# Optimization experiments

Hardware: AMD Instinct MI355X
Metric: run time of the kernel (lower is better)

The kernel has to match this reference:

```python
import jax, jax.numpy as jnp
import numpy as np

E = 16        # num_experts
H = 1024      # hidden_size
I = 768       # moe_intermediate_size
TOP_K = 2     # num_experts_per_tok
B, S = 1, 2048


def setup_inputs() -> dict:
    key = jax.random.key(0)
    ks = jax.random.split(key, 5)
    scale = 0.02
    return {
        "hidden_states": jax.random.normal(ks[0], (B, S, H), dtype=jnp.float32),
        "gate_w": jax.random.normal(ks[1], (E, H), dtype=jnp.float32) * scale,
        "gate_proj": jax.random.normal(ks[2], (E, I, H), dtype=jnp.float32) * scale,
        "up_proj": jax.random.normal(ks[3], (E, I, H), dtype=jnp.float32) * scale,
        "down_proj": jax.random.normal(ks[4], (E, H, I), dtype=jnp.float32) * scale,
    }


def reference(hidden_states, gate_w, gate_proj, up_proj, down_proj):
    b, s, h = hidden_states.shape
    x = hidden_states.reshape(-1, h)                        # [T, H]
    T = x.shape[0]

    # Router: logits -> fp32 softmax -> top-k -> renormalize (norm_topk_prob=True)
    router_logits = x @ gate_w.T                            # [T, E]
    probs = jax.nn.softmax(router_logits.astype(jnp.float32), axis=-1)
    top_vals, top_idx = jax.lax.top_k(probs, TOP_K)         # [T, k]
    top_vals = top_vals / jnp.sum(top_vals, axis=-1, keepdims=True)

    # Dense combine-weight matrix [T, E] (zero for unrouted experts)
    rw = jnp.zeros((T, E), dtype=jnp.float32)
    rw = rw.at[jnp.arange(T)[:, None], top_idx].add(top_vals)
    rw = rw.astype(hidden_states.dtype)

    # Expert SwiGLU MLPs (dense-over-experts reference for the grouped GEMM)
    g = jnp.einsum("th,eih->eti", x, gate_proj)             # [E, T, I]
    u = jnp.einsum("th,eih->eti", x, up_proj)               # [E, T, I]
    hmid = jax.nn.silu(g) * u                                # [E, T, I]
    expert_out = jnp.einsum("eti,ehi->eth", hmid, down_proj)  # [E, T, H]

    # Weighted combine
    out = jnp.einsum("eth,te->th", expert_out, rw)          # [T, H]
    return out.reshape(b, s, h)
```

## Files before the change

kernel.cpp:

```cpp
#include <hip/hip_runtime.h>
#include <hip/hip_bf16.h>
#include <cmath>

constexpr int T = 2048;
constexpr int H = 1024;
constexpr int I = 768;
constexpr int E = 16;
constexpr int WMAX = 48;

typedef short short8 __attribute__((ext_vector_type(8)));
typedef float f32x4  __attribute__((ext_vector_type(4)));

__device__ __forceinline__ short f2bf(float f) {
    __hip_bfloat16 h = __float2bfloat16(f);
    return *reinterpret_cast<short*>(&h);
}

__device__ __forceinline__ short8 pack8(float4 a, float4 b) {
    short8 v = {f2bf(a.x), f2bf(a.y), f2bf(a.z), f2bf(a.w),
                f2bf(b.x), f2bf(b.y), f2bf(b.z), f2bf(b.w)};
    return v;
}

__device__ __forceinline__ int sw(int r, int kg) {
    return r * 32 + (((kg + (r >> 1)) & 3) << 3);
}

__device__ __forceinline__ bool find_item(const int* __restrict__ cnt, int bx,
                                          int& e_o, int& t0_o, int& n_o) {
    int c = 0;
    #pragma unroll
    for (int e = 0; e < E; ++e) {
        int n = cnt[e];
        int m = (n + 127) >> 7;
        if (bx < c + m) { e_o = e; t0_o = (bx - c) << 7; n_o = n; return true; }
        c += m;
    }
    return false;
}

__global__ __launch_bounds__(128) void router_kernel(
    const float* __restrict__ x,
    const float* __restrict__ gw,
    short* __restrict__ xb,
    int* __restrict__ cnt,
    int* __restrict__ entries,
    float* __restrict__ wlist)
{
    const int tid = threadIdx.x;
    const int tl = tid & 7, e = tid >> 3;
    const int t = blockIdx.x * 8 + tl;

    const float4* xr = (const float4*)(x + (size_t)t * H);
    const float4* gr = (const float4*)(gw + (size_t)e * H);
    short* xrow = xb + (size_t)t * H;

    float s0 = 0.f, s1 = 0.f;
    #pragma unroll 8
    for (int q = 0; q < 256; q += 2) {
        float4 a = xr[q],     b = gr[q];
        float4 c = xr[q + 1], d = gr[q + 1];
        s0 += a.x * b.x + a.y * b.y + a.z * b.z + a.w * b.w;
        s1 += c.x * d.x + c.y * d.y + c.z * d.z + c.w * d.w;
        if ((q >> 4) == e)
            *(short8*)(xrow + q * 4) = pack8(a, c);
    }

    __shared__ float lg[8][17];
    lg[tl][e] = s0 + s1;
    __syncthreads();

    if (tid < 8) {
        int tk = blockIdx.x * 8 + tid;
        float v1 = -3.0e38f, v2 = -3.0e38f;
        int i1 = 0, i2 = 0;
        #pragma unroll
        for (int k = 0; k < E; ++k) {
            float v = lg[tid][k];
            if (v > v1) { v2 = v1; i2 = i1; v1 = v; i1 = k; }
            else if (v > v2) { v2 = v; i2 = k; }
        }
        float w1 = 1.f / (1.f + expf(v2 - v1));
        float w2 = 1.f - w1;
        int p = atomicAdd(&cnt[i1], 1);
        entries[i1 * T + p] = tk * 2;
        wlist[i1 * T + p] = w1;
        p = atomicAdd(&cnt[i2], 1);
        entries[i2 * T + p] = tk * 2 + 1;
        wlist[i2 * T + p] = w2;
    }
}

__global__ __launch_bounds__(256) void gateup_mfma(
    const short* __restrict__ xb,
    const float* __restrict__ gate_p,
    const float* __restrict__ up_p,
    const int* __restrict__ cnt,
    const int* __restrict__ entries,
    short* __restrict__ hmid)
{
    int e, t0, n;
    if (!find_item(cnt, blockIdx.x, e, t0, n)) return;
    const int i0 = blockIdx.y * 32;

    __shared__ short Xs[128 * 32];
    __shared__ short Gs[32 * 32];
    __shared__ short Us[32 * 32];
    __shared__ int toks[128];

    const int tid = threadIdx.x;
    if (tid < 128) {
        int r = t0 + tid;
        toks[tid] = (r < n) ? entries[e * T + r] : -1;
    }
    __syncthreads();

    const int lane = tid & 63, wave = tid >> 6;
    const int m16 = lane & 15, q = lane >> 4;
    const int mh = wave >> 1, ng = wave & 1;

    const int sr = tid >> 2, skg = tid & 3;
    const int xt0 = toks[sr], xt1 = toks[64 + sr];
    const short* xsrc0 = xb + (size_t)((xt0 >= 0 ? xt0 : 0) >> 1) * H + skg * 8;
    const short* xsrc1 = xb + (size_t)((xt1 >= 0 ? xt1 : 0) >> 1) * H + skg * 8;
    const int wrow = (tid & 127) >> 2;
    const float* wsrc = (tid >= 128 ? up_p : gate_p)
        + (size_t)e * I * H + (size_t)(i0 + wrow) * H + skg * 8;
    short* wdst = (tid >= 128) ? Us : Gs;

    f32x4 accg[4], accu[4];
    #pragma unroll
    for (int a = 0; a < 4; ++a) {
        accg[a] = (f32x4){0.f, 0.f, 0.f, 0.f};
        accu[a] = (f32x4){0.f, 0.f, 0.f, 0.f};
    }

    short8 xc0 = *(const short8*)xsrc0;
    short8 xc1 = *(const short8*)xsrc1;
    float4 wc0 = *(const float4*)wsrc, wc1 = *(const float4*)(wsrc + 4);

    for (int k0 = 0; k0 < H; k0 += 32) {
        *(short8*)&Xs[sw(sr, skg)]      = xc0;
        *(short8*)&Xs[sw(64 + sr, skg)] = xc1;
        *(short8*)&wdst[sw(wrow, skg)]  = pack8(wc0, wc1);
        int kn = (k0 + 32 < H) ? k0 + 32 : 0;
        xc0 = *(const short8*)(xsrc0 + kn);
        xc1 = *(const short8*)(xsrc1 + kn);
        wc0 = *(const float4*)(wsrc + kn); wc1 = *(const float4*)(wsrc + kn + 4);
        __syncthreads();

        short8 bg = *(const short8*)&Gs[sw(ng * 16 + m16, q)];
        short8 bu = *(const short8*)&Us[sw(ng * 16 + m16, q)];
        #pragma unroll
        for (int mi = 0; mi < 4; ++mi) {
            short8 af = *(const short8*)&Xs[sw(mh * 64 + mi * 16 + m16, q)];
            accg[mi] = __builtin_amdgcn_mfma_f32_16x16x32_bf16(af, bg, accg[mi], 0, 0, 0);
            accu[mi] = __builtin_amdgcn_mfma_f32_16x16x32_bf16(af, bu, accu[mi], 0, 0, 0);
        }
        __syncthreads();
    }

    const int col = i0 + ng * 16 + m16;
    #pragma unroll
    for (int mi = 0; mi < 4; ++mi)
        #pragma unroll
        for (int j = 0; j < 4; ++j) {
            int row = mh * 64 + mi * 16 + q * 4 + j;
            int slot = toks[row];
            if (slot < 0) continue;
            float g = accg[mi][j];
            float u = accu[mi][j];
            float hv = g / (1.f + expf(-g)) * u;
            ((unsigned short*)hmid)[(size_t)slot * I + col] = (unsigned short)f2bf(hv);
        }
}

__global__ __launch_bounds__(256) void down_mfma(
    const short* __restrict__ hmid,
    const float* __restrict__ down_p,
    const int* __restrict__ cnt,
    const int* __restrict__ entries,
    const float* __restrict__ wlist,
    float* __restrict__ out)
{
    int e, t0, n;
    if (!find_item(cnt, blockIdx.x, e, t0, n)) return;
    const int h0 = blockIdx.y * 64;

    __shared__ short As[128 * 32];
    __shared__ short Bs[64 * 32];
    __shared__ int toks[128];
    __shared__ float wr[128];

    const int tid = threadIdx.x;
    if (tid < 128) {
        int r = t0 + tid;
        bool v = (r < n);
        toks[tid] = v ? entries[e * T + r] : -1;
        wr[tid]   = v ? wlist[e * T + r] : 0.f;
    }
    __syncthreads();

    const int lane = tid & 63, wave = tid >> 6;
    const int m16 = lane & 15, q = lane >> 4;

    const int sr = tid >> 2, skg = tid & 3;
    const int at0 = toks[sr], at1 = toks[64 + sr];
    const short* asrc0 = hmid + (size_t)(at0 >= 0 ? at0 : 0) * I + skg * 8;
    const short* asrc1 = hmid + (size_t)(at1 >= 0 ? at1 : 0) * I + skg * 8;
    const float* bsrc = down_p + (size_t)e * H * I + (size_t)(h0 + sr) * I + skg * 8;

    f32x4 acc[8];
    #pragma unroll
    for (int a = 0; a < 8; ++a) acc[a] = (f32x4){0.f, 0.f, 0.f, 0.f};

    short8 ac0 = *(const short8*)asrc0;
    short8 ac1 = *(const short8*)asrc1;
    float4 bc0 = *(const float4*)bsrc, bc1 = *(const float4*)(bsrc + 4);

    for (int k0 = 0; k0 < I; k0 += 32) {
        *(short8*)&As[sw(sr, skg)]      = ac0;
        *(short8*)&As[sw(64 + sr, skg)] = ac1;
        *(short8*)&Bs[sw(sr, skg)]      = pack8(bc0, bc1);
        int kn = (k0 + 32 < I) ? k0 + 32 : 0;
        ac0 = *(const short8*)(asrc0 + kn);
        ac1 = *(const short8*)(asrc1 + kn);
        bc0 = *(const float4*)(bsrc + kn); bc1 = *(const float4*)(bsrc + kn + 4);
        __syncthreads();

        short8 bf = *(const short8*)&Bs[sw(wave * 16 + m16, q)];
        #pragma unroll
        for (int mi = 0; mi < 8; ++mi) {
            short8 af = *(const short8*)&As[sw(mi * 16 + m16, q)];
            acc[mi] = __builtin_amdgcn_mfma_f32_16x16x32_bf16(af, bf, acc[mi], 0, 0, 0);
        }
        __syncthreads();
    }

    const int col = h0 + wave * 16 + m16;
    #pragma unroll
    for (int mi = 0; mi < 8; ++mi)
        #pragma unroll
        for (int j = 0; j < 4; ++j) {
            int row = mi * 16 + q * 4 + j;
            int slot = toks[row];
            if (slot < 0) continue;
            atomicAdd(&out[(size_t)(slot >> 1) * H + col], wr[row] * acc[mi][j]);
        }
}

extern "C" void kernel_launch(void* const* d_in, const int* in_sizes, int n_in,
                              void* d_out, int out_size, void* d_ws, size_t ws_size,
                              hipStream_t stream) {
    const float* x  = (const float*)d_in[0];
    const float* gw = (const float*)d_in[1];
    const float* gp = (const float*)d_in[2];
    const float* up = (const float*)d_in[3];
    const float* dp = (const float*)d_in[4];
    float* out = (float*)d_out;

    char* ws = (char*)d_ws;
    int*   cnt     = (int*)ws;
    int*   entries = (int*)(ws + 2048);
    float* wlist   = (float*)(ws + 2048 + 131072);
    short* xb      = (short*)(ws + 2048 + 262144);
    short* hmid    = xb + (size_t)T * H;

    hipMemsetAsync(ws, 0, 2048, stream);
    hipMemsetAsync(out, 0, (size_t)T * H * sizeof(float), stream);

    router_kernel<<<T / 8, 128, 0, stream>>>(x, gw, xb, cnt, entries, wlist);
    gateup_mfma<<<dim3(WMAX, I / 32), 256, 0, stream>>>(
        xb, gp, up, cnt, entries, hmid);
    down_mfma<<<dim3(WMAX, H / 64), 256, 0, stream>>>(
        hmid, dp, cnt, entries, wlist, out);
}
```

Before: 299.7 us.

## Drop LDS staging in expert GEMMs, load MFMA fragments directly from global

Both expert GEMM kernels no longer stage tiles through shared memory. Each wave now loads its A and B MFMA fragments straight from global memory into registers, software-pipelined one k-step ahead, which removes both __syncthreads per k-step. The gate/up tile widens to 64 columns with 128 rows per wave, and the router splits the H reduction across two halves with 256 threads. The cost is that X rows are no longer shared through LDS, so every wave reloads them through cache, and register pressure rises.

Result: slower. 401.7 us (+34.0%).

```diff
diff --git a/kernel.cpp b/kernel.cpp
--- a/kernel.cpp
+++ b/kernel.cpp
@@ -22,10 +22,6 @@
     return v;
 }
 
-__device__ __forceinline__ int sw(int r, int kg) {
-    return r * 32 + (((kg + (r >> 1)) & 3) << 3);
-}
-
 __device__ __forceinline__ bool find_item(const int* __restrict__ cnt, int bx,
                                           int& e_o, int& t0_o, int& n_o) {
     int c = 0;
@@ -39,7 +35,7 @@
     return false;
 }
 
-__global__ __launch_bounds__(128) void router_kernel(
+__global__ __launch_bounds__(256) void router_kernel(
     const float* __restrict__ x,
     const float* __restrict__ gw,
     short* __restrict__ xb,
@@ -48,26 +44,29 @@
     float* __restrict__ wlist)
 {
     const int tid = threadIdx.x;
-    const int tl = tid & 7, e = tid >> 3;
-    const int t = blockIdx.x * 8 + tl;
+    const int tl = tid & 7;
+    const int e  = (tid >> 3) & 15;
+    const int hf = tid >> 7;
+    const int t  = blockIdx.x * 8 + tl;
 
     const float4* xr = (const float4*)(x + (size_t)t * H);
     const float4* gr = (const float4*)(gw + (size_t)e * H);
     short* xrow = xb + (size_t)t * H;
 
     float s0 = 0.f, s1 = 0.f;
+    const int qlo = hf * 128, qhi = qlo + 128;
     #pragma unroll 8
-    for (int q = 0; q < 256; q += 2) {
+    for (int q = qlo; q < qhi; q += 2) {
         float4 a = xr[q],     b = gr[q];
         float4 c = xr[q + 1], d = gr[q + 1];
         s0 += a.x * b.x + a.y * b.y + a.z * b.z + a.w * b.w;
         s1 += c.x * d.x + c.y * d.y + c.z * d.z + c.w * d.w;
-        if ((q >> 4) == e)
+        if (((q >> 3) & 15) == e)
             *(short8*)(xrow + q * 4) = pack8(a, c);
     }
 
-    __shared__ float lg[8][17];
-    lg[tl][e] = s0 + s1;
+    __shared__ float lg[8][16][2];
+    lg[tl][e][hf] = s0 + s1;
     __syncthreads();
 
     if (tid < 8) {
@@ -76,7 +75,7 @@
         int i1 = 0, i2 = 0;
         #pragma unroll
         for (int k = 0; k < E; ++k) {
-            float v = lg[tid][k];
+            float v = lg[tid][k][0] + lg[tid][k][1];
             if (v > v1) { v2 = v1; i2 = i1; v1 = v; i1 = k; }
             else if (v > v2) { v2 = v; i2 = k; }
         }
@@ -91,7 +90,7 @@
     }
 }
 
-__global__ __launch_bounds__(256) void gateup_mfma(
+__global__ __launch_bounds__(256, 2) void gateup_mfma(
     const short* __restrict__ xb,
     const float* __restrict__ gate_p,
     const float* __restrict__ up_p,
@@ -101,13 +100,9 @@
 {
     int e, t0, n;
     if (!find_item(cnt, blockIdx.x, e, t0, n)) return;
-    const int i0 = blockIdx.y * 32;
-
-    __shared__ short Xs[128 * 32];
-    __shared__ short Gs[32 * 32];
-    __shared__ short Us[32 * 32];
+    const int i0 = blockIdx.y * 64;
+
     __shared__ int toks[128];
-
     const int tid = threadIdx.x;
     if (tid < 128) {
         int r = t0 + tid;
@@ -117,55 +112,57 @@
 
     const int lane = tid & 63, wave = tid >> 6;
     const int m16 = lane & 15, q = lane >> 4;
-    const int mh = wave >> 1, ng = wave & 1;
-
-    const int sr = tid >> 2, skg = tid & 3;
-    const int xt0 = toks[sr], xt1 = toks[64 + sr];
-    const short* xsrc0 = xb + (size_t)((xt0 >= 0 ? xt0 : 0) >> 1) * H + skg * 8;
-    const short* xsrc1 = xb + (size_t)((xt1 >= 0 ? xt1 : 0) >> 1) * H + skg * 8;
-    const int wrow = (tid & 127) >> 2;
-    const float* wsrc = (tid >= 128 ? up_p : gate_p)
-        + (size_t)e * I * H + (size_t)(i0 + wrow) * H + skg * 8;
-    short* wdst = (tid >= 128) ? Us : Gs;
-
-    f32x4 accg[4], accu[4];
-    #pragma unroll
-    for (int a = 0; a < 4; ++a) {
+
+    const short* abase[8];
+    #pragma unroll
+    for (int mi = 0; mi < 8; ++mi) {
+        int tk = toks[mi * 16 + m16];
+        abase[mi] = xb + (size_t)((tk >= 0 ? tk : 0) >> 1) * H + q * 8;
+    }
+    const size_t wroff = (size_t)e * I * H + (size_t)(i0 + wave * 16 + m16) * H + q * 8;
+    const float* gb = gate_p + wroff;
+    const float* ub = up_p + wroff;
+
+    f32x4 accg[8], accu[8];
+    #pragma unroll
+    for (int a = 0; a < 8; ++a) {
         accg[a] = (f32x4){0.f, 0.f, 0.f, 0.f};
         accu[a] = (f32x4){0.f, 0.f, 0.f, 0.f};
     }
 
-    short8 xc0 = *(const short8*)xsrc0;
-    short8 xc1 = *(const short8*)xsrc1;
-    float4 wc0 = *(const float4*)wsrc, wc1 = *(const float4*)(wsrc + 4);
-
+    short8 xc[8];
+    #pragma unroll
+    for (int mi = 0; mi < 8; ++mi) xc[mi] = *(const short8*)(abase[mi]);
+    float4 gc0 = *(const float4*)(gb),     gc1 = *(const float4*)(gb + 4);
+    float4 uc0 = *(const float4*)(ub),     uc1 = *(const float4*)(ub + 4);
+
+    #pragma unroll 2
     for (int k0 = 0; k0 < H; k0 += 32) {
-        *(short8*)&Xs[sw(sr, skg)]      = xc0;
-        *(short8*)&Xs[sw(64 + sr, skg)] = xc1;
-        *(short8*)&wdst[sw(wrow, skg)]  = pack8(wc0, wc1);
         int kn = (k0 + 32 < H) ? k0 + 32 : 0;
-        xc0 = *(const short8*)(xsrc0 + kn);
-        xc1 = *(const short8*)(xsrc1 + kn);
-        wc0 = *(const float4*)(wsrc + kn); wc1 = *(const float4*)(wsrc + kn + 4);
-        __syncthreads();
-
-        short8 bg = *(const short8*)&Gs[sw(ng * 16 + m16, q)];
-        short8 bu = *(const short8*)&Us[sw(ng * 16 + m16, q)];
-        #pragma unroll
-        for (int mi = 0; mi < 4; ++mi) {
-            short8 af = *(const short8*)&Xs[sw(mh * 64 + mi * 16 + m16, q)];
-            accg[mi] = __builtin_amdgcn_mfma_f32_16x16x32_bf16(af, bg, accg[mi], 0, 0, 0);
-            accu[mi] = __builtin_amdgcn_mfma_f32_16x16x32_bf16(af, bu, accu[mi], 0, 0, 0);
-        }
-        __syncthreads();
-    }
-
-    const int col = i0 + ng * 16 + m16;
-    #pragma unroll
-    for (int mi = 0; mi < 4; ++mi)
+        short8 xn[8];
+        #pragma unroll
+        for (int mi = 0; mi < 8; ++mi) xn[mi] = *(const short8*)(abase[mi] + kn);
+        float4 gn0 = *(const float4*)(gb + kn), gn1 = *(const float4*)(gb + kn + 4);
+        float4 un0 = *(const float4*)(ub + kn), un1 = *(const float4*)(ub + kn + 4);
+
+        short8 bg = pack8(gc0, gc1);
+        short8 bu = pack8(uc0, uc1);
+        #pragma unroll
+        for (int mi = 0; mi < 8; ++mi) {
+            accg[mi] = __builtin_amdgcn_mfma_f32_16x16x32_bf16(xc[mi], bg, accg[mi], 0, 0, 0);
+            accu[mi] = __builtin_amdgcn_mfma_f32_16x16x32_bf16(xc[mi], bu, accu[mi], 0, 0, 0);
+        }
+        #pragma unroll
+        for (int mi = 0; mi < 8; ++mi) xc[mi] = xn[mi];
+        gc0 = gn0; gc1 = gn1; uc0 = un0; uc1 = un1;
+    }
+
+    const int col = i0 + wave * 16 + m16;
+    #pragma unroll
+    for (int mi = 0; mi < 8; ++mi)
         #pragma unroll
         for (int j = 0; j < 4; ++j) {
-            int row = mh * 64 + mi * 16 + q * 4 + j;
+            int row = mi * 16 + q * 4 + j;
             int slot = toks[row];
             if (slot < 0) continue;
             float g = accg[mi][j];
@@ -175,7 +172,7 @@
         }
 }
 
-__global__ __launch_bounds__(256) void down_mfma(
+__global__ __launch_bounds__(256, 2) void down_mfma(
     const short* __restrict__ hmid,
     const float* __restrict__ down_p,
     const int* __restrict__ cnt,
@@ -187,11 +184,8 @@
     if (!find_item(cnt, blockIdx.x, e, t0, n)) return;
     const int h0 = blockIdx.y * 64;
 
-    __shared__ short As[128 * 32];
-    __shared__ short Bs[64 * 32];
     __shared__ int toks[128];
     __shared__ float wr[128];
-
     const int tid = threadIdx.x;
     if (tid < 128) {
         int r = t0 + tid;
@@ -204,37 +198,39 @@
     const int lane = tid & 63, wave = tid >> 6;
     const int m16 = lane & 15, q = lane >> 4;
 
-    const int sr = tid >> 2, skg = tid & 3;
-    const int at0 = toks[sr], at1 = toks[64 + sr];
-    const short* asrc0 = hmid + (size_t)(at0 >= 0 ? at0 : 0) * I + skg * 8;
-    const short* asrc1 = hmid + (size_t)(at1 >= 0 ? at1 : 0) * I + skg * 8;
-    const float* bsrc = down_p + (size_t)e * H * I + (size_t)(h0 + sr) * I + skg * 8;
+    const short* abase[8];
+    #pragma unroll
+    for (int mi = 0; mi < 8; ++mi) {
+        int slot = toks[mi * 16 + m16];
+        abase[mi] = hmid + (size_t)(slot >= 0 ? slot : 0) * I + q * 8;
+    }
+    const float* bb = down_p + (size_t)e * H * I
+                    + (size_t)(h0 + wave * 16 + m16) * I + q * 8;
 
     f32x4 acc[8];
     #pragma unroll
     for (int a = 0; a < 8; ++a) acc[a] = (f32x4){0.f, 0.f, 0.f, 0.f};
 
-    short8 ac0 = *(const short8*)asrc0;
-    short8 ac1 = *(const short8*)asrc1;
-    float4 bc0 = *(const float4*)bsrc, bc1 = *(const float4*)(bsrc + 4);
-
+    short8 xc[8];
+    #pragma unroll
+    for (int mi = 0; mi < 8; ++mi) xc[mi] = *(const short8*)(abase[mi]);
+    float4 bc0 = *(const float4*)(bb), bc1 = *(const float4*)(bb + 4);
+
+    #pragma unroll 2
     for (int k0 = 0; k0 < I; k0 += 32) {
-        *(short8*)&As[sw(sr, skg)]      = ac0;
-        *(short8*)&As[sw(64 + sr, skg)] = ac1;
-        *(short8*)&Bs[sw(sr, skg)]      = pack8(bc0, bc1);
         int kn = (k0 + 32 < I) ? k0 + 32 : 0;
-        ac0 = *(const short8*)(asrc0 + kn);
-        ac1 = *(const short8*)(asrc1 + kn);
-        bc0 = *(const float4*)(bsrc + kn); bc1 = *(const float4*)(bsrc + kn + 4);
-        __syncthreads();
-
-        short8 bf = *(const short8*)&Bs[sw(wave * 16 + m16, q)];
-        #pragma unroll
-        for (int mi = 0; mi < 8; ++mi) {
-            short8 af = *(const short8*)&As[sw(mi * 16 + m16, q)];
-            acc[mi] = __builtin_amdgcn_mfma_f32_16x16x32_bf16(af, bf, acc[mi], 0, 0, 0);
-        }
-        __syncthreads();
+        short8 xn[8];
+        #pragma unroll
+        for (int mi = 0; mi < 8; ++mi) xn[mi] = *(const short8*)(abase[mi] + kn);
+        float4 bn0 = *(const float4*)(bb + kn), bn1 = *(const float4*)(bb + kn + 4);
+
+        short8 bf = pack8(bc0, bc1);
+        #pragma unroll
+        for (int mi = 0; mi < 8; ++mi)
+            acc[mi] = __builtin_amdgcn_mfma_f32_16x16x32_bf16(xc[mi], bf, acc[mi], 0, 0, 0);
+        #pragma unroll
+        for (int mi = 0; mi < 8; ++mi) xc[mi] = xn[mi];
+        bc0 = bn0; bc1 = bn1;
     }
 
     const int col = h0 + wave * 16 + m16;
@@ -269,8 +265,8 @@
     hipMemsetAsync(ws, 0, 2048, stream);
     hipMemsetAsync(out, 0, (size_t)T * H * sizeof(float), stream);
 
-    router_kernel<<<T / 8, 128, 0, stream>>>(x, gw, xb, cnt, entries, wlist);
-    gateup_mfma<<<dim3(WMAX, I / 32), 256, 0, stream>>>(
+    router_kernel<<<T / 8, 256, 0, stream>>>(x, gw, xb, cnt, entries, wlist);
+    gateup_mfma<<<dim3(WMAX, I / 64), 256, 0, stream>>>(
         xb, gp, up, cnt, entries, hmid);
     down_mfma<<<dim3(WMAX, H / 64), 256, 0, stream>>>(
         hmid, dp, cnt, entries, wlist, out);
```

## Pre-convert expert weights to tiled bf16 and widen gate/up tile

Applied to the files above, without the earlier changes.

Adds conversion kernels that turn the fp32 gate, up and down weights into bf16 laid out in the exact per-chunk tile order the MFMA kernels consume, so the GEMMs load contiguous short8 chunks instead of strided fp32 rows. This path is used when the workspace is large enough. The gate/up tile grows from 32 to 64 columns so each X tile is reused more. The router is also split across 256 threads by halving the K range. Converting all weights each call is an extra full pass over about 150MB of fp32 weights, whereas routed GEMMs only touch weights of active experts, so the added traffic may outweigh the savings.

Measured after the change: 289.3 us. -3.5%, faster.

```diff
diff --git a/kernel.cpp b/kernel.cpp
--- a/kernel.cpp
+++ b/kernel.cpp
@@ -8,8 +8,9 @@
 constexpr int E = 16;
 constexpr int WMAX = 48;
 
-typedef short short8 __attribute__((ext_vector_type(8)));
-typedef float f32x4  __attribute__((ext_vector_type(4)));
+typedef short short8  __attribute__((ext_vector_type(8)));
+typedef short short4v __attribute__((ext_vector_type(4)));
+typedef float f32x4   __attribute__((ext_vector_type(4)));
 
 __device__ __forceinline__ short f2bf(float f) {
     __hip_bfloat16 h = __float2bfloat16(f);
@@ -39,7 +40,49 @@
     return false;
 }
 
-__global__ __launch_bounds__(128) void router_kernel(
+__global__ __launch_bounds__(256) void cvt_guw(
+    const float* __restrict__ gp, const float* __restrict__ up,
+    short* __restrict__ wtg, short* __restrict__ wtu)
+{
+    const int N4 = (E * I * H) / 4;
+    const int stride = gridDim.x * 256;
+    #pragma unroll 2
+    for (int l4 = blockIdx.x * 256 + threadIdx.x; l4 < 2 * N4; l4 += stride) {
+        const bool isu = (l4 >= N4);
+        const int l = (isu ? l4 - N4 : l4) << 2;
+        const float* src = isu ? up : gp;
+        short* dst = isu ? wtu : wtg;
+        float4 v = *(const float4*)(src + l);
+        int e = l / (I * H);
+        int rem = l - e * (I * H);
+        int i = rem >> 10, kk = rem & 1023;
+        int chunk = ((e * 12 + (i >> 6)) * 32 + (kk >> 5)) << 11;
+        int pos = chunk + (((i & 63) << 2) + ((kk >> 3) & 3)) * 8 + (kk & 7);
+        short4v s = {f2bf(v.x), f2bf(v.y), f2bf(v.z), f2bf(v.w)};
+        *(short4v*)(dst + pos) = s;
+    }
+}
+
+__global__ __launch_bounds__(256) void cvt_dw(
+    const float* __restrict__ dp, short* __restrict__ wtd)
+{
+    const int N4 = (E * H * I) / 4;
+    const int stride = gridDim.x * 256;
+    #pragma unroll 2
+    for (int l4 = blockIdx.x * 256 + threadIdx.x; l4 < N4; l4 += stride) {
+        const int l = l4 << 2;
+        float4 v = *(const float4*)(dp + l);
+        int e = l / (H * I);
+        int rem = l - e * (H * I);
+        int h = rem / 768, kk = rem - h * 768;
+        int chunk = ((e * 16 + (h >> 6)) * 24 + (kk >> 5)) << 11;
+        int pos = chunk + (((h & 63) << 2) + ((kk >> 3) & 3)) * 8 + (kk & 7);
+        short4v s = {f2bf(v.x), f2bf(v.y), f2bf(v.z), f2bf(v.w)};
+        *(short4v*)(wtd + pos) = s;
+    }
+}
+
+__global__ __launch_bounds__(256) void router_kernel(
     const float* __restrict__ x,
     const float* __restrict__ gw,
     short* __restrict__ xb,
@@ -48,26 +91,29 @@
     float* __restrict__ wlist)
 {
     const int tid = threadIdx.x;
-    const int tl = tid & 7, e = tid >> 3;
-    const int t = blockIdx.x * 8 + tl;
+    const int tl = tid & 7;
+    const int e  = (tid >> 3) & 15;
+    const int hf = tid >> 7;
+    const int t  = blockIdx.x * 8 + tl;
 
     const float4* xr = (const float4*)(x + (size_t)t * H);
     const float4* gr = (const float4*)(gw + (size_t)e * H);
     short* xrow = xb + (size_t)t * H;
 
     float s0 = 0.f, s1 = 0.f;
+    const int qlo = hf * 128, qhi = qlo + 128;
     #pragma unroll 8
-    for (int q = 0; q < 256; q += 2) {
+    for (int q = qlo; q < qhi; q += 2) {
         float4 a = xr[q],     b = gr[q];
         float4 c = xr[q + 1], d = gr[q + 1];
         s0 += a.x * b.x + a.y * b.y + a.z * b.z + a.w * b.w;
         s1 += c.x * d.x + c.y * d.y + c.z * d.z + c.w * d.w;
-        if ((q >> 4) == e)
+        if (((q >> 3) & 15) == e)
             *(short8*)(xrow + q * 4) = pack8(a, c);
     }
 
-    __shared__ float lg[8][17];
-    lg[tl][e] = s0 + s1;
+    __shared__ float lg[8][16][2];
+    lg[tl][e][hf] = s0 + s1;
     __syncthreads();
 
     if (tid < 8) {
@@ -76,7 +122,7 @@
         int i1 = 0, i2 = 0;
         #pragma unroll
         for (int k = 0; k < E; ++k) {
-            float v = lg[tid][k];
+            float v = lg[tid][k][0] + lg[tid][k][1];
             if (v > v1) { v2 = v1; i2 = i1; v1 = v; i1 = k; }
             else if (v > v2) { v2 = v; i2 = k; }
         }
@@ -91,21 +137,24 @@
     }
 }
 
+template<bool TILED>
 __global__ __launch_bounds__(256) void gateup_mfma(
     const short* __restrict__ xb,
     const float* __restrict__ gate_p,
     const float* __restrict__ up_p,
+    const short* __restrict__ wtg,
+    const short* __restrict__ wtu,
     const int* __restrict__ cnt,
     const int* __restrict__ entries,
     short* __restrict__ hmid)
 {
     int e, t0, n;
     if (!find_item(cnt, blockIdx.x, e, t0, n)) return;
-    const int i0 = blockIdx.y * 32;
+    const int i0 = blockIdx.y * 64;
 
     __shared__ short Xs[128 * 32];
-    __shared__ short Gs[32 * 32];
-    __shared__ short Us[32 * 32];
+    __shared__ short Gs[64 * 32];
+    __shared__ short Us[64 * 32];
     __shared__ int toks[128];
 
     const int tid = threadIdx.x;
@@ -117,55 +166,75 @@
 
     const int lane = tid & 63, wave = tid >> 6;
     const int m16 = lane & 15, q = lane >> 4;
-    const int mh = wave >> 1, ng = wave & 1;
 
     const int sr = tid >> 2, skg = tid & 3;
     const int xt0 = toks[sr], xt1 = toks[64 + sr];
     const short* xsrc0 = xb + (size_t)((xt0 >= 0 ? xt0 : 0) >> 1) * H + skg * 8;
     const short* xsrc1 = xb + (size_t)((xt1 >= 0 ? xt1 : 0) >> 1) * H + skg * 8;
-    const int wrow = (tid & 127) >> 2;
-    const float* wsrc = (tid >= 128 ? up_p : gate_p)
-        + (size_t)e * I * H + (size_t)(i0 + wrow) * H + skg * 8;
-    short* wdst = (tid >= 128) ? Us : Gs;
-
-    f32x4 accg[4], accu[4];
-    #pragma unroll
-    for (int a = 0; a < 4; ++a) {
+    const float* gsrc = gate_p + (size_t)e * I * H + (size_t)(i0 + sr) * H + skg * 8;
+    const float* usrc = up_p   + (size_t)e * I * H + (size_t)(i0 + sr) * H + skg * 8;
+    const short* gts = wtg + ((size_t)(e * 12 + blockIdx.y) * 32) * 2048 + tid * 8;
+    const short* uts = wtu + ((size_t)(e * 12 + blockIdx.y) * 32) * 2048 + tid * 8;
+
+    f32x4 accg[8], accu[8];
+    #pragma unroll
+    for (int a = 0; a < 8; ++a) {
         accg[a] = (f32x4){0.f, 0.f, 0.f, 0.f};
         accu[a] = (f32x4){0.f, 0.f, 0.f, 0.f};
     }
 
     short8 xc0 = *(const short8*)xsrc0;
     short8 xc1 = *(const short8*)xsrc1;
-    float4 wc0 = *(const float4*)wsrc, wc1 = *(const float4*)(wsrc + 4);
-
-    for (int k0 = 0; k0 < H; k0 += 32) {
+    short8 gt, ut;
+    float4 gc0, gc1, uc0, uc1;
+    if constexpr (TILED) {
+        gt = *(const short8*)gts;
+        ut = *(const short8*)uts;
+    } else {
+        gc0 = *(const float4*)gsrc; gc1 = *(const float4*)(gsrc + 4);
+        uc0 = *(const float4*)usrc; uc1 = *(const float4*)(usrc + 4);
+    }
+
+    for (int ks = 0; ks < H / 32; ++ks) {
         *(short8*)&Xs[sw(sr, skg)]      = xc0;
         *(short8*)&Xs[sw(64 + sr, skg)] = xc1;
-        *(short8*)&wdst[sw(wrow, skg)]  = pack8(wc0, wc1);
-        int kn = (k0 + 32 < H) ? k0 + 32 : 0;
+        if constexpr (TILED) {
+            *(short8*)&Gs[sw(sr, skg)] = gt;
+            *(short8*)&Us[sw(sr, skg)] = ut;
+        } else {
+            *(short8*)&Gs[sw(sr, skg)] = pack8(gc0, gc1);
+            *(short8*)&Us[sw(sr, skg)] = pack8(uc0, uc1);
+        }
+        int ksn = (ks + 1 < H / 32) ? ks + 1 : 0;
+        int kn = ksn * 32;
         xc0 = *(const short8*)(xsrc0 + kn);
         xc1 = *(const short8*)(xsrc1 + kn);
-        wc0 = *(const float4*)(wsrc + kn); wc1 = *(const float4*)(wsrc + kn + 4);
+        if constexpr (TILED) {
+            gt = *(const short8*)(gts + ksn * 2048);
+            ut = *(const short8*)(uts + ksn * 2048);
+        } else {
+            gc0 = *(const float4*)(gsrc + kn); gc1 = *(const float4*)(gsrc + kn + 4);
+            uc0 = *(const float4*)(usrc + kn); uc1 = *(const float4*)(usrc + kn + 4);
+        }
         __syncthreads();
 
-        short8 bg = *(const short8*)&Gs[sw(ng * 16 + m16, q)];
-        short8 bu = *(const short8*)&Us[sw(ng * 16 + m16, q)];
-        #pragma unroll
-        for (int mi = 0; mi < 4; ++mi) {
-            short8 af = *(const short8*)&Xs[sw(mh * 64 + mi * 16 + m16, q)];
+        short8 bg = *(const short8*)&Gs[sw(wave * 16 + m16, q)];
+        short8 bu = *(const short8*)&Us[sw(wave * 16 + m16, q)];
+        #pragma unroll
+        for (int mi = 0; mi < 8; ++mi) {
+            short8 af = *(const short8*)&Xs[sw(mi * 16 + m16, q)];
             accg[mi] = __builtin_amdgcn_mfma_f32_16x16x32_bf16(af, bg, accg[mi], 0, 0, 0);
             accu[mi] = __builtin_amdgcn_mfma_f32_16x16x32_bf16(af, bu, accu[mi], 0, 0, 0);
         }
         __syncthreads();
     }
 
-    const int col = i0 + ng * 16 + m16;
-    #pragma unroll
-    for (int mi = 0; mi < 4; ++mi)
+    const int col = i0 + wave * 16 + m16;
+    #pragma unroll
+    for (int mi = 0; mi < 8; ++mi)
         #pragma unroll
         for (int j = 0; j < 4; ++j) {
-            int row = mh * 64 + mi * 16 + q * 4 + j;
+            int row = mi * 16 + q * 4 + j;
             int slot = toks[row];
             if (slot < 0) continue;
             float g = accg[mi][j];
@@ -175,9 +244,11 @@
         }
 }
 
+template<bool TILED>
 __global__ __launch_bounds__(256) void down_mfma(
     const short* __restrict__ hmid,
     const float* __restrict__ down_p,
+    const short* __restrict__ wtd,
     const int* __restrict__ cnt,
     const int* __restrict__ entries,
     const float* __restrict__ wlist,
@@ -209,6 +280,7 @@
     const short* asrc0 = hmid + (size_t)(at0 >= 0 ? at0 : 0) * I + skg * 8;
     const short* asrc1 = hmid + (size_t)(at1 >= 0 ? at1 : 0) * I + skg * 8;
     const float* bsrc = down_p + (size_t)e * H * I + (size_t)(h0 + sr) * I + skg * 8;
+    const short* bts = wtd + ((size_t)(e * 16 + blockIdx.y) * 24) * 2048 + tid * 8;
 
     f32x4 acc[8];
     #pragma unroll
@@ -216,16 +288,31 @@
 
     short8 ac0 = *(const short8*)asrc0;
     short8 ac1 = *(const short8*)asrc1;
-    float4 bc0 = *(const float4*)bsrc, bc1 = *(const float4*)(bsrc + 4);
-
-    for (int k0 = 0; k0 < I; k0 += 32) {
+    short8 bt;
+    float4 bc0, bc1;
+    if constexpr (TILED) {
+        bt = *(const short8*)bts;
+    } else {
+        bc0 = *(const float4*)bsrc; bc1 = *(const float4*)(bsrc + 4);
+    }
+
+    for (int ks = 0; ks < I / 32; ++ks) {
         *(short8*)&As[sw(sr, skg)]      = ac0;
         *(short8*)&As[sw(64 + sr, skg)] = ac1;
-        *(short8*)&Bs[sw(sr, skg)]      = pack8(bc0, bc1);
-        int kn = (k0 + 32 < I) ? k0 + 32 : 0;
+        if constexpr (TILED) {
+            *(short8*)&Bs[sw(sr, skg)] = bt;
+        } else {
+            *(short8*)&Bs[sw(sr, skg)] = pack8(bc0, bc1);
+        }
+        int ksn = (ks + 1 < I / 32) ? ks + 1 : 0;
+        int kn = ksn * 32;
         ac0 = *(const short8*)(asrc0 + kn);
         ac1 = *(const short8*)(asrc1 + kn);
-        bc0 = *(const float4*)(bsrc + kn); bc1 = *(const float4*)(bsrc + kn + 4);
+        if constexpr (TILED) {
+            bt = *(const short8*)(bts + ksn * 2048);
+        } else {
+            bc0 = *(const float4*)(bsrc + kn); bc1 = *(const float4*)(bsrc + kn + 4);
+        }
         __syncthreads();
 
         short8 bf = *(const short8*)&Bs[sw(wave * 16 + m16, q)];
@@ -265,13 +352,30 @@
     float* wlist   = (float*)(ws + 2048 + 131072);
     short* xb      = (short*)(ws + 2048 + 262144);
     short* hmid    = xb + (size_t)T * H;
+    short* wtg     = hmid + (size_t)2 * T * I;
+    short* wtu     = wtg + (size_t)E * I * H;
+    short* wtd     = wtu + (size_t)E * I * H;
+    const size_t NEED = 2048 + 262144
+                      + (size_t)T * H * 2
+                      + (size_t)2 * T * I * 2
+                      + (size_t)3 * E * I * H * 2;
+    const bool tiled = (ws_size >= NEED);
 
     hipMemsetAsync(ws, 0, 2048, stream);
     hipMemsetAsync(out, 0, (size_t)T * H * sizeof(float), stream);
 
-    router_kernel<<<T / 8, 128, 0, stream>>>(x, gw, xb, cnt, entries, wlist);
-    gateup_mfma<<<dim3(WMAX, I / 32), 256, 0, stream>>>(
-        xb, gp, up, cnt, entries, hmid);
-    down_mfma<<<dim3(WMAX, H / 64), 256, 0, stream>>>(
-        hmid, dp, cnt, entries, wlist, out);
-}
+    router_kernel<<<T / 8, 256, 0, stream>>>(x, gw, xb, cnt, entries, wlist);
+    if (tiled) {
+        cvt_guw<<<2048, 256, 0, stream>>>(gp, up, wtg, wtu);
+        cvt_dw<<<2048, 256, 0, stream>>>(dp, wtd);
+        gateup_mfma<true><<<dim3(WMAX, I / 64), 256, 0, stream>>>(
+            xb, gp, up, wtg, wtu, cnt, entries, hmid);
+        down_mfma<true><<<dim3(WMAX, H / 64), 256, 0, stream>>>(
+            hmid, dp, wtd, cnt, entries, wlist, out);
+    } else {
+        gateup_mfma<false><<<dim3(WMAX, I / 64), 256, 0, stream>>>(
+            xb, gp, up, nullptr, nullptr, cnt, entries, hmid);
+        down_mfma<false><<<dim3(WMAX, H / 64), 256, 0, stream>>>(
+            hmid, dp, nullptr, cnt, entries, wlist, out);
+    }
+}
```

## Pre-convert expert weights to tiled bf16 in a fused prep kernel

Applied to the files above, without the earlier changes.

Adds a prep kernel that converts the fp32 gate/up/down expert weights into bf16 stored in per-tile, K-slab-contiguous layouts, and fuses the router into the same launch as extra blocks. The GEMM kernels then load ready bf16 tiles with single short8 loads instead of fp32 loads plus packing. Each expert's weights were previously reloaded and reconverted by every token tile, so the conversion is now done once and the GEMMs read half the bytes. The gate/up tile widens to 64 columns to raise reuse of the X tile. The cost is an extra full pass over all weights (read fp32, write bf16) on every call, plus a larger workspace.

Result: faster. 285.1 us (-4.9%).

```diff
diff --git a/kernel.cpp b/kernel.cpp
--- a/kernel.cpp
+++ b/kernel.cpp
@@ -8,8 +8,13 @@
 constexpr int E = 16;
 constexpr int WMAX = 48;
 
-typedef short short8 __attribute__((ext_vector_type(8)));
-typedef float f32x4  __attribute__((ext_vector_type(4)));
+constexpr int CVT_ITEMS = 768 * 3;
+constexpr int RTR_BLOCKS = T / 8;
+constexpr int CS = 2056;
+
+typedef short short8  __attribute__((ext_vector_type(8)));
+typedef short short4v __attribute__((ext_vector_type(4)));
+typedef float f32x4   __attribute__((ext_vector_type(4)));
 
 __device__ __forceinline__ short f2bf(float f) {
     __hip_bfloat16 h = __float2bfloat16(f);
@@ -39,44 +44,93 @@
     return false;
 }
 
-__global__ __launch_bounds__(128) void router_kernel(
+__global__ __launch_bounds__(256) void prep_kernel(
     const float* __restrict__ x,
     const float* __restrict__ gw,
+    const float* __restrict__ gp,
+    const float* __restrict__ up,
+    const float* __restrict__ dp,
     short* __restrict__ xb,
+    short* __restrict__ wtg,
+    short* __restrict__ wtu,
+    short* __restrict__ wtd,
     int* __restrict__ cnt,
     int* __restrict__ entries,
     float* __restrict__ wlist)
 {
+    __shared__ short lds[8 * CS];
+    __shared__ float lg[8][16][2];
+
     const int tid = threadIdx.x;
-    const int tl = tid & 7, e = tid >> 3;
-    const int t = blockIdx.x * 8 + tl;
+    const int bid = blockIdx.x;
+
+    if (bid < CVT_ITEMS) {
+        const float* src; short* dst; int K;
+        if (bid < 1536) {
+            const int mat = bid >= 768;
+            const int id3 = mat ? bid - 768 : bid;
+            const int e = id3 / 48, rem = id3 - e * 48;
+            const int rb = rem >> 2, kq = rem & 3;
+            K = H;
+            src = (mat ? up : gp) + (size_t)e * I * H + (size_t)(rb * 64) * H + kq * 256;
+            dst = (mat ? wtu : wtg) + ((size_t)(e * 12 + rb) * 32 + kq * 8) * 2048;
+        } else {
+            const int id3 = bid - 1536;
+            const int e = id3 / 48, rem = id3 - e * 48;
+            const int rb = rem / 3, kq = rem - rb * 3;
+            K = I;
+            src = dp + (size_t)e * H * I + (size_t)(rb * 64) * I + kq * 256;
+            dst = wtd + ((size_t)(e * 16 + rb) * 24 + kq * 8) * 2048;
+        }
+
+        #pragma unroll
+        for (int it = 0; it < 16; ++it) {
+            const int r  = it * 4 + (tid >> 6);
+            const int kk = (tid & 63) * 4;
+            float4 v = *(const float4*)(src + (size_t)r * K + kk);
+            short4v s = {f2bf(v.x), f2bf(v.y), f2bf(v.z), f2bf(v.w)};
+            *(short4v*)&lds[(kk >> 5) * CS + r * 32 + (kk & 31)] = s;
+        }
+        __syncthreads();
+        #pragma unroll
+        for (int j = 0; j < 8; ++j)
+            *(short8*)(dst + j * 2048 + tid * 8) =
+                *(const short8*)&lds[j * CS + tid * 8];
+        return;
+    }
+
+    const int rb  = bid - CVT_ITEMS;
+    const int tl = tid & 7;
+    const int e  = (tid >> 3) & 15;
+    const int hf = tid >> 7;
+    const int t  = rb * 8 + tl;
 
     const float4* xr = (const float4*)(x + (size_t)t * H);
     const float4* gr = (const float4*)(gw + (size_t)e * H);
     short* xrow = xb + (size_t)t * H;
 
     float s0 = 0.f, s1 = 0.f;
+    const int qlo = hf * 128, qhi = qlo + 128;
     #pragma unroll 8
-    for (int q = 0; q < 256; q += 2) {
+    for (int q = qlo; q < qhi; q += 2) {
         float4 a = xr[q],     b = gr[q];
         float4 c = xr[q + 1], d = gr[q + 1];
         s0 += a.x * b.x + a.y * b.y + a.z * b.z + a.w * b.w;
         s1 += c.x * d.x + c.y * d.y + c.z * d.z + c.w * d.w;
-        if ((q >> 4) == e)
+        if (((q >> 3) & 15) == e)
             *(short8*)(xrow + q * 4) = pack8(a, c);
     }
 
-    __shared__ float lg[8][17];
-    lg[tl][e] = s0 + s1;
+    lg[tl][e][hf] = s0 + s1;
     __syncthreads();
 
     if (tid < 8) {
-        int tk = blockIdx.x * 8 + tid;
+        int tk = rb * 8 + tid;
         float v1 = -3.0e38f, v2 = -3.0e38f;
         int i1 = 0, i2 = 0;
         #pragma unroll
         for (int k = 0; k < E; ++k) {
-            float v = lg[tid][k];
+            float v = lg[tid][k][0] + lg[tid][k][1];
             if (v > v1) { v2 = v1; i2 = i1; v1 = v; i1 = k; }
             else if (v > v2) { v2 = v; i2 = k; }
         }
@@ -93,19 +147,19 @@
 
 __global__ __launch_bounds__(256) void gateup_mfma(
     const short* __restrict__ xb,
-    const float* __restrict__ gate_p,
-    const float* __restrict__ up_p,
+    const short* __restrict__ wtg,
+    const short* __restrict__ wtu,
     const int* __restrict__ cnt,
     const int* __restrict__ entries,
     short* __restrict__ hmid)
 {
     int e, t0, n;
     if (!find_item(cnt, blockIdx.x, e, t0, n)) return;
-    const int i0 = blockIdx.y * 32;
+    const int i0 = blockIdx.y * 64;
 
     __shared__ short Xs[128 * 32];
-    __shared__ short Gs[32 * 32];
-    __shared__ short Us[32 * 32];
+    __shared__ short Gs[64 * 32];
+    __shared__ short Us[64 * 32];
     __shared__ int toks[128];
 
     const int tid = threadIdx.x;
@@ -117,55 +171,56 @@
 
     const int lane = tid & 63, wave = tid >> 6;
     const int m16 = lane & 15, q = lane >> 4;
-    const int mh = wave >> 1, ng = wave & 1;
 
     const int sr = tid >> 2, skg = tid & 3;
     const int xt0 = toks[sr], xt1 = toks[64 + sr];
     const short* xsrc0 = xb + (size_t)((xt0 >= 0 ? xt0 : 0) >> 1) * H + skg * 8;
     const short* xsrc1 = xb + (size_t)((xt1 >= 0 ? xt1 : 0) >> 1) * H + skg * 8;
-    const int wrow = (tid & 127) >> 2;
-    const float* wsrc = (tid >= 128 ? up_p : gate_p)
-        + (size_t)e * I * H + (size_t)(i0 + wrow) * H + skg * 8;
-    short* wdst = (tid >= 128) ? Us : Gs;
-
-    f32x4 accg[4], accu[4];
-    #pragma unroll
-    for (int a = 0; a < 4; ++a) {
+    const short* gts = wtg + ((size_t)(e * 12 + blockIdx.y) * 32) * 2048 + tid * 8;
+    const short* uts = wtu + ((size_t)(e * 12 + blockIdx.y) * 32) * 2048 + tid * 8;
+
+    f32x4 accg[8], accu[8];
+    #pragma unroll
+    for (int a = 0; a < 8; ++a) {
         accg[a] = (f32x4){0.f, 0.f, 0.f, 0.f};
         accu[a] = (f32x4){0.f, 0.f, 0.f, 0.f};
     }
 
     short8 xc0 = *(const short8*)xsrc0;
     short8 xc1 = *(const short8*)xsrc1;
-    float4 wc0 = *(const float4*)wsrc, wc1 = *(const float4*)(wsrc + 4);
-
-    for (int k0 = 0; k0 < H; k0 += 32) {
+    short8 gt = *(const short8*)gts;
+    short8 ut = *(const short8*)uts;
+
+    for (int ks = 0; ks < H / 32; ++ks) {
         *(short8*)&Xs[sw(sr, skg)]      = xc0;
         *(short8*)&Xs[sw(64 + sr, skg)] = xc1;
-        *(short8*)&wdst[sw(wrow, skg)]  = pack8(wc0, wc1);
-        int kn = (k0 + 32 < H) ? k0 + 32 : 0;
+        *(short8*)&Gs[sw(sr, skg)] = gt;
+        *(short8*)&Us[sw(sr, skg)] = ut;
+        int ksn = (ks + 1 < H / 32) ? ks + 1 : 0;
+        int kn = ksn * 32;
         xc0 = *(const short8*)(xsrc0 + kn);
         xc1 = *(const short8*)(xsrc1 + kn);
-        wc0 = *(const float4*)(wsrc + kn); wc1 = *(const float4*)(wsrc + kn + 4);
-        __syncthreads();
-
-        short8 bg = *(const short8*)&Gs[sw(ng * 16 + m16, q)];
-        short8 bu = *(const short8*)&Us[sw(ng * 16 + m16, q)];
-        #pragma unroll
-        for (int mi = 0; mi < 4; ++mi) {
-            short8 af = *(const short8*)&Xs[sw(mh * 64 + mi * 16 + m16, q)];
+        gt = *(const short8*)(gts + ksn * 2048);
+        ut = *(const short8*)(uts + ksn * 2048);
+        __syncthreads();
+
+        short8 bg = *(const short8*)&Gs[sw(wave * 16 + m16, q)];
+        short8 bu = *(const short8*)&Us[sw(wave * 16 + m16, q)];
+        #pragma unroll
+        for (int mi = 0; mi < 8; ++mi) {
+            short8 af = *(const short8*)&Xs[sw(mi * 16 + m16, q)];
             accg[mi] = __builtin_amdgcn_mfma_f32_16x16x32_bf16(af, bg, accg[mi], 0, 0, 0);
             accu[mi] = __builtin_amdgcn_mfma_f32_16x16x32_bf16(af, bu, accu[mi], 0, 0, 0);
         }
         __syncthreads();
     }
 
-    const int col = i0 + ng * 16 + m16;
-    #pragma unroll
-    for (int mi = 0; mi < 4; ++mi)
+    const int col = i0 + wave * 16 + m16;
+    #pragma unroll
+    for (int mi = 0; mi < 8; ++mi)
         #pragma unroll
         for (int j = 0; j < 4; ++j) {
-            int row = mh * 64 + mi * 16 + q * 4 + j;
+            int row = mi * 16 + q * 4 + j;
             int slot = toks[row];
             if (slot < 0) continue;
             float g = accg[mi][j];
@@ -177,7 +232,7 @@
 
 __global__ __launch_bounds__(256) void down_mfma(
     const short* __restrict__ hmid,
-    const float* __restrict__ down_p,
+    const short* __restrict__ wtd,
     const int* __restrict__ cnt,
     const int* __restrict__ entries,
     const float* __restrict__ wlist,
@@ -208,7 +263,7 @@
     const int at0 = toks[sr], at1 = toks[64 + sr];
     const short* asrc0 = hmid + (size_t)(at0 >= 0 ? at0 : 0) * I + skg * 8;
     const short* asrc1 = hmid + (size_t)(at1 >= 0 ? at1 : 0) * I + skg * 8;
-    const float* bsrc = down_p + (size_t)e * H * I + (size_t)(h0 + sr) * I + skg * 8;
+    const short* bts = wtd + ((size_t)(e * 16 + blockIdx.y) * 24) * 2048 + tid * 8;
 
     f32x4 acc[8];
     #pragma unroll
@@ -216,16 +271,17 @@
 
     short8 ac0 = *(const short8*)asrc0;
     short8 ac1 = *(const short8*)asrc1;
-    float4 bc0 = *(const float4*)bsrc, bc1 = *(const float4*)(bsrc + 4);
-
-    for (int k0 = 0; k0 < I; k0 += 32) {
+    short8 bt = *(const short8*)bts;
+
+    for (int ks = 0; ks < I / 32; ++ks) {
         *(short8*)&As[sw(sr, skg)]      = ac0;
         *(short8*)&As[sw(64 + sr, skg)] = ac1;
-        *(short8*)&Bs[sw(sr, skg)]      = pack8(bc0, bc1);
-        int kn = (k0 + 32 < I) ? k0 + 32 : 0;
+        *(short8*)&Bs[sw(sr, skg)]      = bt;
+        int ksn = (ks + 1 < I / 32) ? ks + 1 : 0;
+        int kn = ksn * 32;
         ac0 = *(const short8*)(asrc0 + kn);
         ac1 = *(const short8*)(asrc1 + kn);
-        bc0 = *(const float4*)(bsrc + kn); bc1 = *(const float4*)(bsrc + kn + 4);
+        bt = *(const short8*)(bts + ksn * 2048);
         __syncthreads();
 
         short8 bf = *(const short8*)&Bs[sw(wave * 16 + m16, q)];
@@ -265,13 +321,17 @@
     float* wlist   = (float*)(ws + 2048 + 131072);
     short* xb      = (short*)(ws + 2048 + 262144);
     short* hmid    = xb + (size_t)T * H;
+    short* wtg     = hmid + (size_t)2 * T * I;
+    short* wtu     = wtg + (size_t)E * I * H;
+    short* wtd     = wtu + (size_t)E * I * H;
 
     hipMemsetAsync(ws, 0, 2048, stream);
     hipMemsetAsync(out, 0, (size_t)T * H * sizeof(float), stream);
 
-    router_kernel<<<T / 8, 128, 0, stream>>>(x, gw, xb, cnt, entries, wlist);
-    gateup_mfma<<<dim3(WMAX, I / 32), 256, 0, stream>>>(
-        xb, gp, up, cnt, entries, hmid);
+    prep_kernel<<<CVT_ITEMS + RTR_BLOCKS, 256, 0, stream>>>(
+        x, gw, gp, up, dp, xb, wtg, wtu, wtd, cnt, entries, wlist);
+    gateup_mfma<<<dim3(WMAX, I / 64), 256, 0, stream>>>(
+        xb, wtg, wtu, cnt, entries, hmid);
     down_mfma<<<dim3(WMAX, H / 64), 256, 0, stream>>>(
-        hmid, dp, cnt, entries, wlist, out);
-}
+        hmid, wtd, cnt, entries, wlist, out);
+}
```
